# Performance work log

Measured on AMD Instinct MI355X. Metric: run time of the kernel, lower is better.

Reference implementation:

```python
import jax, jax.numpy as jnp
import numpy as np


def setup_inputs() -> dict:
    key = jax.random.key(0)
    k0, k1, k2, k3, k4 = jax.random.split(key, 5)
    dim, b, h, w = 256, 32, 56, 56
    x = jax.random.normal(k0, (b, dim, h, w), jnp.float32)
    # 1x1 conv qk: weight [out=dim, in=dim], bias [dim]
    qk_w = jax.random.normal(k1, (dim, dim), jnp.float32) * (1.0 / np.sqrt(dim))
    qk_b = jax.random.normal(k2, (dim,), jnp.float32) * 0.01
    # depthwise 3x3 conv pe: weight [dim, 1, 3, 3], bias [dim]
    pe_w = jax.random.normal(k3, (dim, 1, 3, 3), jnp.float32) * (1.0 / 3.0)
    pe_b = jax.random.normal(k4, (dim,), jnp.float32) * 0.01
    return {"x": x, "qk_w": qk_w, "qk_b": qk_b, "pe_w": pe_w, "pe_b": pe_b}


def reference(x, qk_w, qk_b, pe_w, pe_b):
    b, c, h, w = x.shape
    n = h * w
    d = c // 2                      # head_dim = dim // 2
    s = float(n) ** -0.5
    # 1x1 conv + (elu + 1) feature map
    qk = jnp.einsum('bchw,oc->bohw', x, qk_w) + qk_b[None, :, None, None]
    qk = jax.nn.elu(qk) + 1.0
    qk = qk.reshape(b, 2, d, n)
    q, k = qk[:, 0], qk[:, 1]       # each [b, d, n]
    v = x.reshape(b, c, n)          # [b, c, n]
    # kv outer product: (k*s) @ (v^T * s) -> [b, d, c]
    kv = jnp.einsum('bdn,bcn->bdc', k, v) * (s * s)
    # numerator q^T @ kv -> [b, n, c]
    num = jnp.einsum('bdn,bdc->bnc', q, kv)
    # denominator q^T @ mean(k, axis=-1) -> [b, n, 1]
    den = jnp.einsum('bdn,bd->bn', q, jnp.mean(k, axis=-1))[:, :, None] + 1e-6
    attn = (num / den).transpose(0, 2, 1).reshape(b, c, h, w)
    # depthwise 3x3 positional conv on v (= x)
    pe = jax.lax.conv_general_dilated(
        x, pe_w, window_strides=(1, 1), padding='SAME',
        dimension_numbers=('NCHW', 'OIHW', 'NCHW'), feature_group_count=c)
    return attn + pe + pe_b[None, :, None, None]
```

## Files before the change

### kernel.cpp

```cpp
#include <hip/hip_runtime.h>

#define B_ 32
#define C_ 256
#define D_ 128
#define HH 56
#define WW 56
#define N_ 3136
#define KSPLIT 7
#define KRANGE 448

typedef float f32x4 __attribute__((ext_vector_type(4)));
typedef short s16x8 __attribute__((ext_vector_type(8)));
typedef unsigned short u16x8 __attribute__((ext_vector_type(8)));

__device__ __forceinline__ int swz4(int r){
  return (r & 3) ^ (((r >> 2) & 1) << 1) ^ ((r >> 3) & 1);
}
__device__ __forceinline__ unsigned short f2bf(float f){
  unsigned u = __float_as_uint(f);
  u += 0x7fffu + ((u >> 16) & 1u);
  return (unsigned short)(u >> 16);
}
__device__ __forceinline__ float bf2f(unsigned short h){
  return __uint_as_float(((unsigned)h) << 16);
}
__device__ __forceinline__ float elu1(float v){
  return v > 0.f ? v + 1.f : __expf(v);
}
__device__ __forceinline__ unsigned cvtpk(float lo, float hi){
  unsigned r;
  asm("v_cvt_pk_bf16_f32 %0, %1, %2" : "=v"(r) : "v"(lo), "v"(hi));
  return r;
}

template<int R>
__device__ __forceinline__ void stage_glds(const unsigned short* gp, int ld, char* lds){
  const int tid = threadIdx.x;
  const int wid = tid >> 6;
#pragma unroll
  for (int q = 0; q < R/64; ++q){
    const int slot = q*256 + tid;
    const int r = slot >> 2, gi = slot & 3;
    const int u = gi ^ swz4(r);
    const unsigned short* ga = gp + r*ld + u*8;
    char* lb = lds + (q*256 + wid*64)*16;
    __builtin_amdgcn_global_load_lds(
        (__attribute__((address_space(1))) void*)ga,
        (__attribute__((address_space(3))) void*)lb, 16, 0, 0);
  }
}

__device__ __forceinline__ s16x8 ldsfrag(const char* lds, int r, int g){
  return *(const s16x8*)(lds + r*64 + ((g ^ swz4(r)) << 4));
}

__global__ __launch_bounds__(256) void k0_w(
    const float* __restrict__ w, unsigned short* __restrict__ wb)
{
  const int i = blockIdx.x*256 + threadIdx.x;
  float4 v = *(const float4*)(w + (size_t)i*4);
  uint2 h = {cvtpk(v.x, v.y), cvtpk(v.z, v.w)};
  *(uint2*)(wb + (size_t)i*4) = h;
}

__global__ __launch_bounds__(256) void k0_t(
    const float* __restrict__ x, unsigned short* __restrict__ xt)
{
  __shared__ float T[64][65];
  const int tid = threadIdx.x;
  const int n0 = blockIdx.x*64, c0 = blockIdx.y*64, b = blockIdx.z;
  const float* xb = x + ((size_t)b*C_ + c0)*N_ + n0;
#pragma unroll
  for (int q = 0; q < 4; ++q){
    const int cr = q*16 + (tid >> 4), nc = (tid & 15)*4;
    float4 v = *(const float4*)(xb + (size_t)cr*N_ + nc);
    T[cr][nc+0] = v.x; T[cr][nc+1] = v.y; T[cr][nc+2] = v.z; T[cr][nc+3] = v.w;
  }
  __syncthreads();
  const int nn = tid >> 2, cq = tid & 3;
  unsigned h[8];
#pragma unroll
  for (int j = 0; j < 8; ++j)
    h[j] = cvtpk(T[cq*16 + 2*j][nn], T[cq*16 + 2*j + 1][nn]);
  unsigned short* dst = xt + ((size_t)b*N_ + n0 + nn)*C_ + c0 + cq*16;
  *(uint4*)dst       = (uint4){h[0], h[1], h[2], h[3]};
  *(uint4*)(dst + 8) = (uint4){h[4], h[5], h[6], h[7]};
}

__global__ __launch_bounds__(256) void k1_qk(
    const unsigned short* __restrict__ xt, const unsigned short* __restrict__ wb,
    const float* __restrict__ bias,
    unsigned short* __restrict__ kbuf, unsigned short* __restrict__ qt)
{
  __shared__ __align__(16) char Al[256*64];
  __shared__ __align__(16) char Bl[64*64];
  const int tid = threadIdx.x, lane = tid & 63, wid = tid >> 6;
  const int n0 = blockIdx.x * 64;
  const int b  = blockIdx.y;
  const unsigned short* xtb = xt + ((size_t)b*N_ + n0)*C_;
  const int wo = wid*64;
  f32x4 acc[4][4] = {};

  for (int k0 = 0; k0 < C_; k0 += 32){
    __syncthreads();
    stage_glds<256>(wb + k0, C_, Al);
    stage_glds<64>(xtb + k0, C_, Bl);
    __syncthreads();
    s16x8 af[4], bv4[4];
#pragma unroll
    for (int m = 0; m < 4; ++m)  af[m]  = ldsfrag(Al, wo + m*16 + (lane & 15), lane >> 4);
#pragma unroll
    for (int nf = 0; nf < 4; ++nf) bv4[nf] = ldsfrag(Bl, nf*16 + (lane & 15), lane >> 4);
#pragma unroll
    for (int m = 0; m < 4; ++m)
#pragma unroll
      for (int nf = 0; nf < 4; ++nf)
        acc[m][nf] = __builtin_amdgcn_mfma_f32_16x16x32_bf16(af[m], bv4[nf], acc[m][nf], 0, 0, 0);
  }

  const int col = lane & 15, rg = lane >> 4;
  if (wid < 2){
#pragma unroll
    for (int m = 0; m < 4; ++m){
      const int db = wo + m*16 + rg*4;
      const float b0 = bias[db], b1 = bias[db+1], b2 = bias[db+2], b3 = bias[db+3];
#pragma unroll
      for (int nf = 0; nf < 4; ++nf){
        const int n = n0 + nf*16 + col;
        f32x4 a = acc[m][nf];
        uint2 hv = {cvtpk(elu1(a[0]+b0), elu1(a[1]+b1)),
                    cvtpk(elu1(a[2]+b2), elu1(a[3]+b3))};
        *(uint2*)(qt + ((size_t)b*N_ + n)*D_ + db) = hv;
      }
    }
  } else {
#pragma unroll
    for (int m = 0; m < 4; ++m)
#pragma unroll
      for (int j = 0; j < 4; ++j){
        const int d = wo - 128 + m*16 + rg*4 + j;
        const float bb = bias[128 + d];
#pragma unroll
        for (int nf = 0; nf < 4; ++nf){
          const int n = n0 + nf*16 + col;
          kbuf[((size_t)b*D_ + d)*N_ + n] = f2bf(elu1(acc[m][nf][j] + bb));
        }
      }
  }
}

__global__ __launch_bounds__(256) void k2_kv(
    const unsigned short* __restrict__ kbuf, const float* __restrict__ x,
    unsigned short* __restrict__ kvp, float* __restrict__ kmp)
{
  __shared__ __align__(16) char Al[128*64];
  __shared__ __align__(16) char Bl[256*64];
  const int tid = threadIdx.x, lane = tid & 63, wid = tid >> 6;
  const int ks = blockIdx.x;
  const int b  = blockIdx.y;
  const unsigned short* kb = kbuf + (size_t)b*D_*N_ + ks*KRANGE;
  const float* xb = x + (size_t)b*C_*N_ + ks*KRANGE;
  const int wd = (wid >> 1)*64, wc = (wid & 1)*128;
  f32x4 acc[4][8] = {};
  float kms = 0.f;

  for (int t = 0; t < KRANGE/32; ++t){
    __syncthreads();
    stage_glds<128>(kb + t*32, N_, Al);
#pragma unroll
    for (int q = 0; q < 8; ++q){
      int idx = q*256 + tid;
      int cc = idx >> 3, n4 = (idx & 7)*4;
      float4 v = *(const float4*)(xb + (size_t)cc*N_ + t*32 + n4);
      uint2 h = {cvtpk(v.x, v.y), cvtpk(v.z, v.w)};
      *(uint2*)(Bl + cc*64 + ((n4*2) ^ (swz4(cc) << 4))) = h;
    }
    __syncthreads();
    s16x8 af[4], bv[8];
#pragma unroll
    for (int m = 0; m < 4; ++m)  af[m] = ldsfrag(Al, wd + m*16 + (lane & 15), lane >> 4);
#pragma unroll
    for (int cf = 0; cf < 8; ++cf) bv[cf] = ldsfrag(Bl, wc + cf*16 + (lane & 15), lane >> 4);
#pragma unroll
    for (int m = 0; m < 4; ++m)
#pragma unroll
      for (int cf = 0; cf < 8; ++cf)
        acc[m][cf] = __builtin_amdgcn_mfma_f32_16x16x32_bf16(af[m], bv[cf], acc[m][cf], 0, 0, 0);
    {
      const int dr = tid >> 1, half = tid & 1;
      const char* base = Al + dr*64;
      const int s = swz4(dr);
      uint4 u0 = *(const uint4*)(base + (((half*2 + 0) ^ s) << 4));
      uint4 u1 = *(const uint4*)(base + (((half*2 + 1) ^ s) << 4));
      const unsigned ua[8] = {u0.x,u0.y,u0.z,u0.w,u1.x,u1.y,u1.z,u1.w};
#pragma unroll
      for (int i = 0; i < 8; ++i){
        kms += bf2f((unsigned short)(ua[i] & 0xffffu));
        kms += bf2f((unsigned short)(ua[i] >> 16));
      }
    }
  }

  kms += __shfl_xor(kms, 1);
  if ((tid & 1) == 0) kmp[((size_t)b*KSPLIT + ks)*D_ + (tid >> 1)] = kms;

  const int col = lane & 15, rg = lane >> 4;
#pragma unroll
  for (int m = 0; m < 4; ++m)
#pragma unroll
    for (int j = 0; j < 4; ++j){
      const int d = wd + m*16 + rg*4 + j;
#pragma unroll
      for (int cf = 0; cf < 8; ++cf){
        const int c = wc + cf*16 + col;
        kvp[(((size_t)b*KSPLIT + ks)*D_ + d)*C_ + c] = f2bf(acc[m][cf][j]);
      }
    }
}

__global__ __launch_bounds__(256) void kr_reduce(
    const unsigned short* __restrict__ kvp, const float* __restrict__ kmp,
    unsigned short* __restrict__ kvt, float* __restrict__ km)
{
  __shared__ float T[64][65];
  const int tid = threadIdx.x;
  const int ct = blockIdx.x, dt = blockIdx.y, b = blockIdx.z;
  const int d0 = dt*64, c0 = ct*64;
  const int r = tid >> 2, cq = (tid & 3)*16;
  float v[16] = {};
  for (int j = 0; j < KSPLIT; ++j){
    const unsigned short* p = kvp + (((size_t)b*KSPLIT + j)*D_ + d0 + r)*C_ + c0 + cq;
#pragma unroll
    for (int i = 0; i < 16; ++i) v[i] += bf2f(p[i]);
  }
  const float sc = 1.0f/(float)N_;
#pragma unroll
  for (int i = 0; i < 16; ++i) T[r][cq + i] = v[i]*sc;
  __syncthreads();
  u16x8 h0, h1;
#pragma unroll
  for (int i = 0; i < 8; ++i) h0[i] = f2bf(T[cq + i][r]);
#pragma unroll
  for (int i = 0; i < 8; ++i) h1[i] = f2bf(T[cq + 8 + i][r]);
  unsigned short* o = kvt + ((size_t)b*C_ + c0 + r)*D_ + d0 + cq;
  *(u16x8*)o = h0;
  *(u16x8*)(o + 8) = h1;
  if (ct == 0 && dt == 0 && tid < D_){
    float s = 0.f;
    for (int j = 0; j < KSPLIT; ++j) s += kmp[((size_t)b*KSPLIT + j)*D_ + tid];
    km[b*D_ + tid] = s*sc;
  }
}

__global__ __launch_bounds__(256) void k3_attn(
    const unsigned short* __restrict__ qt, const unsigned short* __restrict__ kvt,
    const float* __restrict__ km, unsigned short* __restrict__ attn)
{
  __shared__ __align__(16) char SM[256*64 + 64*64];
  char* Al = SM;
  char* Bl = SM + 256*64;
  unsigned short* P = (unsigned short*)SM;
  __shared__ float kms[128];
  __shared__ float dens[64];
  const int tid = threadIdx.x, lane = tid & 63, wid = tid >> 6;
  const int n0 = blockIdx.x * 64;
  const int b  = blockIdx.y;
  if (tid < 128) kms[tid] = km[b*D_ + tid];
  const unsigned short* kvb = kvt + (size_t)b*C_*D_;
  const unsigned short* qtb = qt + ((size_t)b*N_ + n0)*D_;
  const int wc = wid*64;
  f32x4 acc[4][4] = {};
  float den = 0.f;

  for (int k0 = 0; k0 < D_; k0 += 32){
    __syncthreads();
    stage_glds<256>(kvb + k0, D_, Al);
    stage_glds<64>(qtb + k0, D_, Bl);
    __syncthreads();
    s16x8 af[4], bv4[4];
#pragma unroll
    for (int m = 0; m < 4; ++m)  af[m]  = ldsfrag(Al, wc + m*16 + (lane & 15), lane >> 4);
#pragma unroll
    for (int nf = 0; nf < 4; ++nf) bv4[nf] = ldsfrag(Bl, nf*16 + (lane & 15), lane >> 4);
#pragma unroll
    for (int m = 0; m < 4; ++m)
#pragma unroll
      for (int nf = 0; nf < 4; ++nf)
        acc[m][nf] = __builtin_amdgcn_mfma_f32_16x16x32_bf16(af[m], bv4[nf], acc[m][nf], 0, 0, 0);
    {
      const int nr = tid >> 2, g = tid & 3;
      uint4 u = *(const uint4*)(Bl + nr*64 + ((g ^ swz4(nr)) << 4));
      const float* kp = kms + k0 + g*8;
      const unsigned ua[4] = {u.x, u.y, u.z, u.w};
#pragma unroll
      for (int i = 0; i < 4; ++i){
        den += bf2f((unsigned short)(ua[i] & 0xffffu)) * kp[i*2];
        den += bf2f((unsigned short)(ua[i] >> 16))     * kp[i*2 + 1];
      }
    }
  }
  den += __shfl_xor(den, 1);
  den += __shfl_xor(den, 2);
  if ((tid & 3) == 0) dens[tid >> 2] = den;
  __syncthreads();

  const int col = lane & 15, rg = lane >> 4;
  float rdv[4];
#pragma unroll
  for (int nf = 0; nf < 4; ++nf)
    rdv[nf] = 1.0f / (dens[nf*16 + col] + 1e-6f);

#pragma unroll
  for (int h = 0; h < 2; ++h){
    if ((wid >> 1) == h){
      const int lc = wc - h*128;
#pragma unroll
      for (int m = 0; m < 4; ++m)
#pragma unroll
        for (int nf = 0; nf < 4; ++nf)
#pragma unroll
          for (int j = 0; j < 4; ++j)
            P[(lc + m*16 + rg*4 + j)*72 + (nf*16 + col)] = f2bf(acc[m][nf][j] * rdv[nf]);
    }
    __syncthreads();
#pragma unroll
    for (int p = 0; p < 4; ++p){
      const int c = (tid >> 3) + p*32, ch = tid & 7;
      u16x8 v = *(const u16x8*)(P + c*72 + ch*8);
      *(u16x8*)(attn + ((size_t)b*C_ + h*128 + c)*N_ + n0 + ch*8) = v;
    }
    __syncthreads();
  }
}

__global__ __launch_bounds__(256) void k4_pe(
    const float* __restrict__ x, const unsigned short* __restrict__ attn,
    const float* __restrict__ pw, const float* __restrict__ pb,
    float* __restrict__ out)
{
  __shared__ float xs_raw[58*56 + 8];
  float* xs = xs_raw + 4;
  const int tid = threadIdx.x;
  const int ch = blockIdx.x, b = blockIdx.y;
  const float* xp = x + ((size_t)b*C_ + ch)*N_;
  if (tid < 14)      ((float4*)xs)[tid] = (float4){0.f,0.f,0.f,0.f};
  else if (tid < 28) ((float4*)xs)[784 + tid] = (float4){0.f,0.f,0.f,0.f};
  for (int i = tid; i < 784; i += 256)
    ((float4*)xs)[14 + i] = ((const float4*)xp)[i];
  const float* wp = pw + ch*9;
  float wgt[9];
#pragma unroll
  for (int i = 0; i < 9; ++i) wgt[i] = wp[i];
  const float bias = pb[ch];
  __syncthreads();
  const unsigned short* ap = attn + ((size_t)b*C_ + ch)*N_;
  float* op = out + ((size_t)b*C_ + ch)*N_;
  for (int u = tid; u < 784; u += 256) {
    const int row = u / 14, g = u - row*14;
    float o0 = bias, o1 = bias, o2 = bias, o3 = bias;
#pragma unroll
    for (int rr = 0; rr < 3; ++rr){
      const float* rp = xs + (row + rr)*56 + g*4;
      float4 cv = *(const float4*)rp;
      float lf = (g > 0)  ? rp[-1] : 0.f;
      float rt = (g < 13) ? rp[4]  : 0.f;
      const float wl = wgt[rr*3], wc_ = wgt[rr*3+1], wr = wgt[rr*3+2];
      o0 += wl*lf   + wc_*cv.x + wr*cv.y;
      o1 += wl*cv.x + wc_*cv.y + wr*cv.z;
      o2 += wl*cv.y + wc_*cv.z + wr*cv.w;
      o3 += wl*cv.z + wc_*cv.w + wr*rt;
    }
    ushort4 av = *(const ushort4*)(ap + u*4);
    float4 ov = {o0 + bf2f(av.x), o1 + bf2f(av.y), o2 + bf2f(av.z), o3 + bf2f(av.w)};
    *(float4*)(op + u*4) = ov;
  }
}

extern "C" void kernel_launch(void* const* d_in, const int* in_sizes, int n_in,
                              void* d_out, int out_size, void* d_ws, size_t ws_size,
                              hipStream_t stream) {
  (void)in_sizes; (void)n_in; (void)out_size; (void)ws_size;
  const float* x   = (const float*)d_in[0];
  const float* qkw = (const float*)d_in[1];
  const float* qkb = (const float*)d_in[2];
  const float* pew = (const float*)d_in[3];
  const float* peb = (const float*)d_in[4];
  float* out = (float*)d_out;

  unsigned short* xts  = (unsigned short*)d_ws;
  unsigned short* kbuf = xts + (size_t)B_*N_*C_;
  unsigned short* qt   = kbuf + (size_t)B_*D_*N_;
  unsigned short* kvt  = qt   + (size_t)B_*N_*D_;
  float* km  = (float*)(kvt + (size_t)B_*C_*D_);
  unsigned short* wb   = kvt;
  unsigned short* kvp  = xts;
  float* kmp = (float*)(kvp + (size_t)B_*KSPLIT*D_*C_);
  unsigned short* attn = xts;

  k0_w     <<<dim3(64),                 256, 0, stream>>>(qkw, wb);
  k0_t     <<<dim3(N_/64, C_/64, B_),   256, 0, stream>>>(x, xts);
  k1_qk    <<<dim3(N_/64, B_),          256, 0, stream>>>(xts, wb, qkb, kbuf, qt);
  k2_kv    <<<dim3(KSPLIT, B_),         256, 0, stream>>>(kbuf, x, kvp, kmp);
  kr_reduce<<<dim3(4, 2, B_),           256, 0, stream>>>(kvp, kmp, kvt, km);
  k3_attn  <<<dim3(N_/64, B_),          256, 0, stream>>>(qt, kvt, km, attn);
  k4_pe    <<<dim3(C_, B_),             256, 0, stream>>>(x, attn, pew, peb, out);
}
```

Baseline: 172.5 us.

## Use 512-thread kv blocks and store partials transposed to simplify reduction

The kv-accumulation kernel now runs 8 waves per block instead of 4, so each wave holds a 64x64 accumulator tile instead of 64x128, which halves register pressure and spreads the 224-block grid across more waves. Its partial results are written transposed in [c][d] order as 4-wide vector stores, so the reduce kernel becomes a plain vectorized sum with no LDS transpose. This trades more threads per block and different staging code for lower per-thread work and simpler partial stores and reduction.

Result: no change. 170.3 us (-1.3%).

```diff
diff --git a/kernel.cpp b/kernel.cpp
--- a/kernel.cpp
+++ b/kernel.cpp
@@ -149,7 +149,7 @@
   }
 }
 
-__global__ __launch_bounds__(256) void k2_kv(
+__global__ __launch_bounds__(512) void k2_kv(
     const unsigned short* __restrict__ kbuf, const float* __restrict__ x,
     unsigned short* __restrict__ kvp, float* __restrict__ kmp)
 {
@@ -160,41 +160,46 @@
   const int b  = blockIdx.y;
   const unsigned short* kb = kbuf + (size_t)b*D_*N_ + ks*KRANGE;
   const float* xb = x + (size_t)b*C_*N_ + ks*KRANGE;
-  const int wd = (wid >> 1)*64, wc = (wid & 1)*128;
-  f32x4 acc[4][8] = {};
+  const int wd = (wid >> 2)*64, wc = (wid & 3)*64;
+  f32x4 acc[4][4] = {};
   float kms = 0.f;
+  const int sr = tid >> 2, sg = tid & 3;
 
   for (int t = 0; t < KRANGE/32; ++t){
     __syncthreads();
-    stage_glds<128>(kb + t*32, N_, Al);
-#pragma unroll
-    for (int q = 0; q < 8; ++q){
-      int idx = q*256 + tid;
+    {
+      const int u = sg ^ swz4(sr);
+      const unsigned short* ga = kb + (size_t)sr*N_ + t*32 + u*8;
+      char* lb = Al + (wid*64)*16;
+      __builtin_amdgcn_global_load_lds(
+          (__attribute__((address_space(1))) void*)ga,
+          (__attribute__((address_space(3))) void*)lb, 16, 0, 0);
+    }
+#pragma unroll
+    for (int q = 0; q < 4; ++q){
+      int idx = q*512 + tid;
       int cc = idx >> 3, n4 = (idx & 7)*4;
       float4 v = *(const float4*)(xb + (size_t)cc*N_ + t*32 + n4);
       uint2 h = {cvtpk(v.x, v.y), cvtpk(v.z, v.w)};
       *(uint2*)(Bl + cc*64 + ((n4*2) ^ (swz4(cc) << 4))) = h;
     }
     __syncthreads();
-    s16x8 af[4], bv[8];
+    s16x8 af[4], bv[4];
 #pragma unroll
     for (int m = 0; m < 4; ++m)  af[m] = ldsfrag(Al, wd + m*16 + (lane & 15), lane >> 4);
 #pragma unroll
-    for (int cf = 0; cf < 8; ++cf) bv[cf] = ldsfrag(Bl, wc + cf*16 + (lane & 15), lane >> 4);
+    for (int cf = 0; cf < 4; ++cf) bv[cf] = ldsfrag(Bl, wc + cf*16 + (lane & 15), lane >> 4);
 #pragma unroll
     for (int m = 0; m < 4; ++m)
 #pragma unroll
-      for (int cf = 0; cf < 8; ++cf)
+      for (int cf = 0; cf < 4; ++cf)
         acc[m][cf] = __builtin_amdgcn_mfma_f32_16x16x32_bf16(af[m], bv[cf], acc[m][cf], 0, 0, 0);
     {
-      const int dr = tid >> 1, half = tid & 1;
-      const char* base = Al + dr*64;
-      const int s = swz4(dr);
-      uint4 u0 = *(const uint4*)(base + (((half*2 + 0) ^ s) << 4));
-      uint4 u1 = *(const uint4*)(base + (((half*2 + 1) ^ s) << 4));
-      const unsigned ua[8] = {u0.x,u0.y,u0.z,u0.w,u1.x,u1.y,u1.z,u1.w};
-#pragma unroll
-      for (int i = 0; i < 8; ++i){
+      uint2 u = *(const uint2*)(Al + sr*64 + ((sg ^ swz4(sr)) << 4));
+      uint2 u2 = *(const uint2*)(Al + sr*64 + ((sg ^ swz4(sr)) << 4) + 8);
+      const unsigned ua[4] = {u.x, u.y, u2.x, u2.y};
+#pragma unroll
+      for (int i = 0; i < 4; ++i){
         kms += bf2f((unsigned short)(ua[i] & 0xffffu));
         kms += bf2f((unsigned short)(ua[i] >> 16));
       }
@@ -202,52 +207,48 @@
   }
 
   kms += __shfl_xor(kms, 1);
-  if ((tid & 1) == 0) kmp[((size_t)b*KSPLIT + ks)*D_ + (tid >> 1)] = kms;
+  kms += __shfl_xor(kms, 2);
+  if ((tid & 3) == 0) kmp[((size_t)b*KSPLIT + ks)*D_ + sr] = kms;
 
   const int col = lane & 15, rg = lane >> 4;
 #pragma unroll
-  for (int m = 0; m < 4; ++m)
-#pragma unroll
-    for (int j = 0; j < 4; ++j){
-      const int d = wd + m*16 + rg*4 + j;
-#pragma unroll
-      for (int cf = 0; cf < 8; ++cf){
-        const int c = wc + cf*16 + col;
-        kvp[(((size_t)b*KSPLIT + ks)*D_ + d)*C_ + c] = f2bf(acc[m][cf][j]);
-      }
-    }
+  for (int m = 0; m < 4; ++m){
+    const int d0 = wd + m*16 + rg*4;
+#pragma unroll
+    for (int cf = 0; cf < 4; ++cf){
+      const int c = wc + cf*16 + col;
+      ushort4 hv = {f2bf(acc[m][cf][0]), f2bf(acc[m][cf][1]),
+                    f2bf(acc[m][cf][2]), f2bf(acc[m][cf][3])};
+      *(ushort4*)(kvp + (((size_t)b*KSPLIT + ks)*C_ + c)*D_ + d0) = hv;
+    }
+  }
 }
 
 __global__ __launch_bounds__(256) void kr_reduce(
     const unsigned short* __restrict__ kvp, const float* __restrict__ kmp,
     unsigned short* __restrict__ kvt, float* __restrict__ km)
 {
-  __shared__ float T[64][65];
   const int tid = threadIdx.x;
-  const int ct = blockIdx.x, dt = blockIdx.y, b = blockIdx.z;
-  const int d0 = dt*64, c0 = ct*64;
-  const int r = tid >> 2, cq = (tid & 3)*16;
-  float v[16] = {};
-  for (int j = 0; j < KSPLIT; ++j){
-    const unsigned short* p = kvp + (((size_t)b*KSPLIT + j)*D_ + d0 + r)*C_ + c0 + cq;
-#pragma unroll
-    for (int i = 0; i < 16; ++i) v[i] += bf2f(p[i]);
-  }
+  const int bx = blockIdx.x, b = blockIdx.y;
   const float sc = 1.0f/(float)N_;
 #pragma unroll
-  for (int i = 0; i < 16; ++i) T[r][cq + i] = v[i]*sc;
-  __syncthreads();
-  u16x8 h0, h1;
-#pragma unroll
-  for (int i = 0; i < 8; ++i) h0[i] = f2bf(T[cq + i][r]);
-#pragma unroll
-  for (int i = 0; i < 8; ++i) h1[i] = f2bf(T[cq + 8 + i][r]);
-  unsigned short* o = kvt + ((size_t)b*C_ + c0 + r)*D_ + d0 + cq;
-  *(u16x8*)o = h0;
-  *(u16x8*)(o + 8) = h1;
-  if (ct == 0 && dt == 0 && tid < D_){
+  for (int it = 0; it < 2; ++it){
+    const int idx = (bx*2 + it)*256 + tid;
+    const int c = idx >> 4, dq = (idx & 15)*8;
+    float s[8] = {};
+    for (int ks = 0; ks < KSPLIT; ++ks){
+      u16x8 v = *(const u16x8*)(kvp + (((size_t)b*KSPLIT + ks)*C_ + c)*D_ + dq);
+#pragma unroll
+      for (int i = 0; i < 8; ++i) s[i] += bf2f(v[i]);
+    }
+    u16x8 h;
+#pragma unroll
+    for (int i = 0; i < 8; ++i) h[i] = f2bf(s[i]*sc);
+    *(u16x8*)(kvt + ((size_t)b*C_ + c)*D_ + dq) = h;
+  }
+  if (bx == 0 && tid < D_){
     float s = 0.f;
-    for (int j = 0; j < KSPLIT; ++j) s += kmp[((size_t)b*KSPLIT + j)*D_ + tid];
+    for (int ks = 0; ks < KSPLIT; ++ks) s += kmp[((size_t)b*KSPLIT + ks)*D_ + tid];
     km[b*D_ + tid] = s*sc;
   }
 }
@@ -400,8 +401,8 @@
   k0_w     <<<dim3(64),                 256, 0, stream>>>(qkw, wb);
   k0_t     <<<dim3(N_/64, C_/64, B_),   256, 0, stream>>>(x, xts);
   k1_qk    <<<dim3(N_/64, B_),          256, 0, stream>>>(xts, wb, qkb, kbuf, qt);
-  k2_kv    <<<dim3(KSPLIT, B_),         256, 0, stream>>>(kbuf, x, kvp, kmp);
-  kr_reduce<<<dim3(4, 2, B_),           256, 0, stream>>>(kvp, kmp, kvt, km);
+  k2_kv    <<<dim3(KSPLIT, B_),         512, 0, stream>>>(kbuf, x, kvp, kmp);
+  kr_reduce<<<dim3(8, B_),              256, 0, stream>>>(kvp, kmp, kvt, km);
   k3_attn  <<<dim3(N_/64, B_),          256, 0, stream>>>(qt, kvt, km, attn);
   k4_pe    <<<dim3(C_, B_),             256, 0, stream>>>(x, attn, pew, peb, out);
 }
```
